# Optimization experiments

Hardware: AMD Instinct MI355X
Metric: run time of the kernel (lower is better)

## Reference

```python
import jax, jax.numpy as jnp
import numpy as np
import math

DIM = 1024
NUM_HEADS = 16
HEAD_DIM = 64
SEQ_LEN = 2048
ATTN_SCALE = 0.12


def cosine_norm(x, eps=1e-12):
    # unit-normalize along last dim
    return x * jax.lax.rsqrt(jnp.sum(x * x, axis=-1, keepdims=True) + eps)


def rotary_tables(T, head_dim):
    dim_quarter = max(1, head_dim // 4)
    angular_freq = (1.0 / 1024.0) ** jnp.linspace(0.0, 1.0, dim_quarter, dtype=jnp.float32)
    angular_freq = jnp.concatenate([angular_freq, jnp.zeros(dim_quarter, dtype=jnp.float32)])  # [head_dim//2]
    t = jnp.arange(T, dtype=jnp.float32)
    theta = t[:, None] * angular_freq[None, :]  # [T, head_dim//2]
    return jnp.cos(theta), jnp.sin(theta)


def apply_rotary(x_BTHD, cos, sin):
    # cos/sin: [T, head_dim//2] -> broadcast [1, T, 1, head_dim//2]
    c = cos[None, :, None, :]
    s = sin[None, :, None, :]
    x1, x2 = jnp.split(x_BTHD, 2, axis=-1)
    y1 = x1 * c + x2 * s
    y2 = -x1 * s + x2 * c
    return jnp.concatenate([y1, y2], axis=-1)


def setup_inputs() -> dict:
    key = jax.random.key(0)
    ks = jax.random.split(key, 6)
    x = jax.random.normal(ks[0], (1, SEQ_LEN, DIM), dtype=jnp.float32)
    init_std = 0.02
    Wq = jax.random.normal(ks[1], (DIM, NUM_HEADS * HEAD_DIM), dtype=jnp.float32) * init_std
    Wk = jax.random.normal(ks[2], (DIM, NUM_HEADS * HEAD_DIM), dtype=jnp.float32) * init_std
    Wv = jax.random.normal(ks[3], (DIM, NUM_HEADS * HEAD_DIM), dtype=jnp.float32) * init_std
    Wo = jax.random.normal(ks[4], (NUM_HEADS * HEAD_DIM, DIM), dtype=jnp.float32) * init_std
    # Scale param: initialized as ones * (1/sqrt(dim)); use rand around that magnitude
    s_qk = jax.random.uniform(ks[5], (NUM_HEADS, HEAD_DIM), dtype=jnp.float32,
                              minval=0.5, maxval=1.5) * (1.0 / math.sqrt(DIM))
    return {"x": x, "Wq": Wq, "Wk": Wk, "Wv": Wv, "Wo": Wo, "s_qk": s_qk}


def reference(x, Wq, Wk, Wv, Wo, s_qk):
    B, T, _ = x.shape
    # projections
    q = (x @ Wq).reshape(B, T, NUM_HEADS, HEAD_DIM)
    k = (x @ Wk).reshape(B, T, NUM_HEADS, HEAD_DIM)
    v = (x @ Wv).reshape(B, T, NUM_HEADS, HEAD_DIM)
    # effective scale: s * (init/scale) with init=1, scale=1/sqrt(dim)
    s_eff = s_qk * math.sqrt(DIM)  # [H, D]
    q = cosine_norm(q) * s_eff[None, None, :, :]
    k = cosine_norm(k) * s_eff[None, None, :, :]
    cos, sin = rotary_tables(T, HEAD_DIM)
    q = apply_rotary(q, cos, sin)
    k = apply_rotary(k, cos, sin)
    # causal attention with fixed scale 0.12 (block_mask == causal)
    scores = jnp.einsum('bthd,bshd->bhts', q, k) * ATTN_SCALE  # [B,H,T,T]
    causal = jnp.tril(jnp.ones((T, T), dtype=bool))
    scores = jnp.where(causal[None, None, :, :], scores, jnp.float32(-1e30))
    attn = jax.nn.softmax(scores, axis=-1)
    y = jnp.einsum('bhts,bshd->bthd', attn, v)
    y = y.reshape(B, T, NUM_HEADS * HEAD_DIM)
    return y @ Wo
```

## Files before the change

### kernel.cpp

```cpp
#include <hip/hip_runtime.h>

typedef unsigned short u16;
typedef unsigned int u32;
typedef __attribute__((ext_vector_type(8))) short bf16x8;
typedef __attribute__((ext_vector_type(4))) float f32x4;

__device__ __forceinline__ u16 f2bf(float x) {
  unsigned u = __float_as_uint(x);
  u += 0x7fffu + ((u >> 16) & 1u);
  return (u16)(u >> 16);
}
__device__ __forceinline__ float bf2f(u16 z) {
  return __uint_as_float((u32)z << 16);
}

__global__ __launch_bounds__(256) void prep(const float* __restrict__ x,
                                            const float* __restrict__ W0,
                                            const float* __restrict__ W1,
                                            const float* __restrict__ W2,
                                            const float* __restrict__ W3,
                                            u16* __restrict__ xb,
                                            u16* __restrict__ Wt,
                                            float2* __restrict__ rtab) {
  __shared__ alignas(16) u16 ls[64 * 72];
  int b = blockIdx.x;
  int tid = threadIdx.x;
  if (b < 2048) {
    int g = b * 256 + tid;
    int i = g * 4;
    float4 f = *(const float4*)(x + i);
    ushort4 o;
    o.x = f2bf(f.x); o.y = f2bf(f.y); o.z = f2bf(f.z); o.w = f2bf(f.w);
    *(ushort4*)(xb + i) = o;
    if (g < 2048 * 16) {
      int t = g >> 4, ii = g & 15;
      float fr = exp2f(-10.0f * (float)ii / 15.0f);
      float th = (float)t * fr;
      rtab[g] = make_float2(cosf(th), sinf(th));
    }
    return;
  }
  int bb = b - 2048;
  int z = bb >> 8;
  int rem = bb & 255;
  const float* W = (z == 0) ? W0 : (z == 1) ? W1 : (z == 2) ? W2 : W3;
  u16* o = Wt + (size_t)z * (1024u * 1024u);
  int kt = (rem >> 4) * 64, nt = (rem & 15) * 64;
  int r = tid >> 2, c0 = (tid & 3) * 16;
  const float* src = W + (size_t)(kt + r) * 1024 + nt + c0;
  u16 tmp[16];
#pragma unroll
  for (int c = 0; c < 16; c += 4) {
    float4 f = *(const float4*)(src + c);
    tmp[c + 0] = f2bf(f.x); tmp[c + 1] = f2bf(f.y);
    tmp[c + 2] = f2bf(f.z); tmp[c + 3] = f2bf(f.w);
  }
#pragma unroll
  for (int c = 0; c < 16; ++c) ls[r * 72 + c0 + c] = tmp[c];
  __syncthreads();
#pragma unroll
  for (int pass = 0; pass < 4; ++pass) {
    int n = pass * 16 + (tid >> 4);
    int kk = (tid & 15) * 4;
    ushort4 val;
    val.x = ls[(kk + 0) * 72 + n];
    val.y = ls[(kk + 1) * 72 + n];
    val.z = ls[(kk + 2) * 72 + n];
    val.w = ls[(kk + 3) * 72 + n];
    *(ushort4*)(o + (size_t)(nt + n) * 1024 + kt + kk) = val;
  }
}

#define GLD 40

__global__ __launch_bounds__(256) void gemm_qkv(const u16* __restrict__ A,
                                                const u16* __restrict__ Wt,
                                                u16* __restrict__ qb,
                                                u16* __restrict__ kb,
                                                u16* __restrict__ vt,
                                                const float* __restrict__ s_qk,
                                                const float2* __restrict__ rtab) {
  __shared__ alignas(16) u16 As[128 * GLD];
  __shared__ alignas(16) u16 Bs[128 * GLD];
  int z = blockIdx.z;
  const u16* B = Wt + (size_t)z * (1024u * 1024u);
  int tid = threadIdx.x;
  int bm = blockIdx.y * 128, bn = blockIdx.x * 128;
  int lane = tid & 63, w = tid >> 6;
  int wm = (w >> 1) * 64, wn = (w & 1) * 64;
  int m16 = lane & 15, q = lane >> 4;
  f32x4 acc[4][4] = {};
  int srow = tid >> 1, scol = (tid & 1) * 16;
  const u16* aptr = A + (size_t)(bm + srow) * 1024 + scol;
  const u16* bptr = B + (size_t)(bn + srow) * 1024 + scol;
  uint4 a0 = *(const uint4*)(aptr);
  uint4 a1 = *(const uint4*)(aptr + 8);
  uint4 b0 = *(const uint4*)(bptr);
  uint4 b1 = *(const uint4*)(bptr + 8);
  for (int k0 = 0; k0 < 1024; k0 += 32) {
    __syncthreads();
    *(uint4*)&As[srow * GLD + scol] = a0;
    *(uint4*)&As[srow * GLD + scol + 8] = a1;
    *(uint4*)&Bs[srow * GLD + scol] = b0;
    *(uint4*)&Bs[srow * GLD + scol + 8] = b1;
    uint4 na0, na1, nb0, nb1;
    if (k0 < 992) {
      na0 = *(const uint4*)(aptr + k0 + 32);
      na1 = *(const uint4*)(aptr + k0 + 40);
      nb0 = *(const uint4*)(bptr + k0 + 32);
      nb1 = *(const uint4*)(bptr + k0 + 40);
    }
    __syncthreads();
    bf16x8 af[4], bfr[4];
#pragma unroll
    for (int mt = 0; mt < 4; ++mt)
      af[mt] = *(const bf16x8*)&As[(wm + mt * 16 + m16) * GLD + q * 8];
#pragma unroll
    for (int nt = 0; nt < 4; ++nt)
      bfr[nt] = *(const bf16x8*)&Bs[(wn + nt * 16 + m16) * GLD + q * 8];
#pragma unroll
    for (int mt = 0; mt < 4; ++mt)
#pragma unroll
      for (int nt = 0; nt < 4; ++nt)
        acc[mt][nt] = __builtin_amdgcn_mfma_f32_16x16x32_bf16(af[mt], bfr[nt], acc[mt][nt], 0, 0, 0);
    if (k0 < 992) { a0 = na0; a1 = na1; b0 = nb0; b1 = nb1; }
  }
  int hh = (bn + wn) >> 6;
  if (z == 2) {
#pragma unroll
    for (int nt = 0; nt < 4; ++nt) {
      int n = bn + wn + nt * 16 + m16;
#pragma unroll
      for (int mt = 0; mt < 4; ++mt) {
        int t0 = bm + wm + mt * 16 + q * 4;
        ushort4 val;
        val.x = f2bf(acc[mt][nt][0]);
        val.y = f2bf(acc[mt][nt][1]);
        val.z = f2bf(acc[mt][nt][2]);
        val.w = f2bf(acc[mt][nt][3]);
        *(ushort4*)(vt + (size_t)n * 2048 + t0) = val;
      }
    }
  } else {
    u16* dst = z ? kb : qb;
    float se0 = s_qk[hh * 64 +  0 + m16] * 32.0f;
    float se1 = s_qk[hh * 64 + 16 + m16] * 32.0f;
    float se2 = s_qk[hh * 64 + 32 + m16] * 32.0f;
    float se3 = s_qk[hh * 64 + 48 + m16] * 32.0f;
#pragma unroll
    for (int mt = 0; mt < 4; ++mt)
#pragma unroll
      for (int r = 0; r < 4; ++r) {
        float ss = acc[mt][0][r] * acc[mt][0][r] + acc[mt][1][r] * acc[mt][1][r]
                 + acc[mt][2][r] * acc[mt][2][r] + acc[mt][3][r] * acc[mt][3][r];
        ss += __shfl_xor(ss, 1); ss += __shfl_xor(ss, 2);
        ss += __shfl_xor(ss, 4); ss += __shfl_xor(ss, 8);
        float inv = rsqrtf(ss + 1e-12f);
        int t = bm + wm + mt * 16 + q * 4 + r;
        float2 cs = rtab[t * 16 + m16];
        float x0 = acc[mt][0][r] * inv * se0;
        float x1 = acc[mt][1][r] * inv * se1;
        float x2 = acc[mt][2][r] * inv * se2;
        float x3 = acc[mt][3][r] * inv * se3;
        size_t off = (size_t)t * 1024 + hh * 64 + m16;
        dst[off]      = f2bf(x0 * cs.x + x2 * cs.y);
        dst[off + 16] = f2bf(x1);
        dst[off + 32] = f2bf(x2 * cs.x - x0 * cs.y);
        dst[off + 48] = f2bf(x3);
      }
  }
}

#define ALD 72
__global__ __launch_bounds__(256) void attn_flash(const u16* __restrict__ qb,
                                                  const u16* __restrict__ kb,
                                                  const u16* __restrict__ vt,
                                                  u16* __restrict__ yb) {
  __shared__ alignas(16) u16 Ks[64 * ALD];
  __shared__ alignas(16) u16 Vt[64 * ALD];
  __shared__ alignas(16) u16 Ps[4 * 16 * ALD];
  int h = blockIdx.x;
  int qt = 31 - blockIdx.y;
  int t0 = qt * 64;
  int tid = threadIdx.x;
  int lane = tid & 63, w = tid >> 6;
  int m16 = lane & 15, q = lane >> 4;
  int krow_s = tid >> 2, kcol_s = (tid & 3) * 16;
  const u16* kbase = kb + (size_t)krow_s * 1024 + h * 64 + kcol_s;
  const u16* vbase = vt + (size_t)(h * 64 + krow_s) * 2048 + kcol_s;
  u16* pw = &Ps[w * 16 * ALD];
  const u16* qrow = qb + (size_t)(t0 + w * 16 + m16) * 1024 + h * 64;
  bf16x8 qa0 = *(const bf16x8*)(qrow + q * 8);
  bf16x8 qa1 = *(const bf16x8*)(qrow + 32 + q * 8);
  f32x4 Yacc[4] = {};
  float lsum[4] = {0.f, 0.f, 0.f, 0.f};
  int trow = t0 + w * 16 + q * 4;
  uint4 kv0 = *(const uint4*)kbase;
  uint4 kv1 = *(const uint4*)(kbase + 8);
  uint4 vv0 = *(const uint4*)vbase;
  uint4 vv1 = *(const uint4*)(vbase + 8);
  for (int jt = 0; jt <= qt; ++jt) {
    __syncthreads();
    *(uint4*)&Ks[krow_s * ALD + kcol_s] = kv0;
    *(uint4*)&Ks[krow_s * ALD + kcol_s + 8] = kv1;
    *(uint4*)&Vt[krow_s * ALD + kcol_s] = vv0;
    *(uint4*)&Vt[krow_s * ALD + kcol_s + 8] = vv1;
    uint4 kn0, kn1, vn0, vn1;
    if (jt < qt) {
      const u16* kp = kbase + (size_t)(jt + 1) * 65536;
      const u16* vp = vbase + (jt + 1) * 64;
      kn0 = *(const uint4*)kp;
      kn1 = *(const uint4*)(kp + 8);
      vn0 = *(const uint4*)vp;
      vn1 = *(const uint4*)(vp + 8);
    }
    __syncthreads();
    f32x4 S[4] = {};
#pragma unroll
    for (int nt = 0; nt < 4; ++nt) {
      bf16x8 b0 = *(const bf16x8*)&Ks[(nt * 16 + m16) * ALD + q * 8];
      bf16x8 b1 = *(const bf16x8*)&Ks[(nt * 16 + m16) * ALD + 32 + q * 8];
      S[nt] = __builtin_amdgcn_mfma_f32_16x16x32_bf16(qa0, b0, S[nt], 0, 0, 0);
      S[nt] = __builtin_amdgcn_mfma_f32_16x16x32_bf16(qa1, b1, S[nt], 0, 0, 0);
    }
    bool diag = (jt == qt);
    int j0 = jt * 64;
    float tmp[4] = {0.f, 0.f, 0.f, 0.f};
#pragma unroll
    for (int nt = 0; nt < 4; ++nt) {
      int j = j0 + nt * 16 + m16;
#pragma unroll
      for (int r = 0; r < 4; ++r) {
        float p = __builtin_amdgcn_exp2f(S[nt][r] * 0.17312340490667562f);
        if (diag && (j > trow + r)) p = 0.f;
        tmp[r] += p;
        pw[(q * 4 + r) * ALD + nt * 16 + m16] = f2bf(p);
      }
    }
#pragma unroll
    for (int r = 0; r < 4; ++r) {
      float s = tmp[r];
      s += __shfl_xor(s, 1); s += __shfl_xor(s, 2);
      s += __shfl_xor(s, 4); s += __shfl_xor(s, 8);
      lsum[r] += s;
    }
    bf16x8 pa0 = *(const bf16x8*)&pw[m16 * ALD + q * 8];
    bf16x8 pa1 = *(const bf16x8*)&pw[m16 * ALD + 32 + q * 8];
#pragma unroll
    for (int nt = 0; nt < 4; ++nt) {
      bf16x8 b0 = *(const bf16x8*)&Vt[(nt * 16 + m16) * ALD + q * 8];
      bf16x8 b1 = *(const bf16x8*)&Vt[(nt * 16 + m16) * ALD + 32 + q * 8];
      Yacc[nt] = __builtin_amdgcn_mfma_f32_16x16x32_bf16(pa0, b0, Yacc[nt], 0, 0, 0);
      Yacc[nt] = __builtin_amdgcn_mfma_f32_16x16x32_bf16(pa1, b1, Yacc[nt], 0, 0, 0);
    }
    if (jt < qt) { kv0 = kn0; kv1 = kn1; vv0 = vn0; vv1 = vn1; }
  }
#pragma unroll
  for (int r = 0; r < 4; ++r) {
    float inv = __builtin_amdgcn_rcpf(lsum[r]);
    int t = t0 + w * 16 + q * 4 + r;
#pragma unroll
    for (int nt = 0; nt < 4; ++nt)
      yb[(size_t)t * 1024 + h * 64 + nt * 16 + m16] = f2bf(Yacc[nt][r] * inv);
  }
}

__global__ __launch_bounds__(256) void gemm_o(const u16* __restrict__ A,
                                              const u16* __restrict__ B,
                                              float* __restrict__ C) {
  __shared__ alignas(16) u16 As[128 * GLD];
  __shared__ alignas(16) u16 Bs[64 * GLD];
  int tid = threadIdx.x;
  int bm = blockIdx.y * 128, bn = blockIdx.x * 64;
  int lane = tid & 63, w = tid >> 6;
  int wm = w * 32;
  int m16 = lane & 15, q = lane >> 4;
  f32x4 acc[2][4] = {};
  int srA = tid >> 1, scA = (tid & 1) * 16;
  int srB = tid >> 2, scB = (tid & 3) * 8;
  const u16* aptr = A + (size_t)(bm + srA) * 1024 + scA;
  const u16* bptr = B + (size_t)(bn + srB) * 1024 + scB;
  uint4 a0 = *(const uint4*)(aptr);
  uint4 a1 = *(const uint4*)(aptr + 8);
  uint4 b0 = *(const uint4*)(bptr);
  for (int k0 = 0; k0 < 1024; k0 += 32) {
    __syncthreads();
    *(uint4*)&As[srA * GLD + scA] = a0;
    *(uint4*)&As[srA * GLD + scA + 8] = a1;
    *(uint4*)&Bs[srB * GLD + scB] = b0;
    uint4 na0, na1, nb0;
    if (k0 < 992) {
      na0 = *(const uint4*)(aptr + k0 + 32);
      na1 = *(const uint4*)(aptr + k0 + 40);
      nb0 = *(const uint4*)(bptr + k0 + 32);
    }
    __syncthreads();
    bf16x8 af[2], bfr[4];
#pragma unroll
    for (int mt = 0; mt < 2; ++mt)
      af[mt] = *(const bf16x8*)&As[(wm + mt * 16 + m16) * GLD + q * 8];
#pragma unroll
    for (int nt = 0; nt < 4; ++nt)
      bfr[nt] = *(const bf16x8*)&Bs[(nt * 16 + m16) * GLD + q * 8];
#pragma unroll
    for (int mt = 0; mt < 2; ++mt)
#pragma unroll
      for (int nt = 0; nt < 4; ++nt)
        acc[mt][nt] = __builtin_amdgcn_mfma_f32_16x16x32_bf16(af[mt], bfr[nt], acc[mt][nt], 0, 0, 0);
    if (k0 < 992) { a0 = na0; a1 = na1; b0 = nb0; }
  }
#pragma unroll
  for (int mt = 0; mt < 2; ++mt)
#pragma unroll
    for (int nt = 0; nt < 4; ++nt)
#pragma unroll
      for (int r = 0; r < 4; ++r) {
        int row = bm + wm + mt * 16 + q * 4 + r;
        int col = bn + nt * 16 + m16;
        C[(size_t)row * 1024 + col] = acc[mt][nt][r];
      }
}

extern "C" void kernel_launch(void* const* d_in, const int* in_sizes, int n_in,
                              void* d_out, int out_size, void* d_ws, size_t ws_size,
                              hipStream_t stream) {
  const float* x   = (const float*)d_in[0];
  const float* Wq  = (const float*)d_in[1];
  const float* Wk  = (const float*)d_in[2];
  const float* Wv  = (const float*)d_in[3];
  const float* Wo  = (const float*)d_in[4];
  const float* sqk = (const float*)d_in[5];
  float* out = (float*)d_out;
  char* ws = (char*)d_ws;

  u16*    xb   = (u16*)ws;
  u16*    Wt   = (u16*)(ws + ((size_t)4 << 20));
  float2* rtab = (float2*)(ws + ((size_t)12 << 20));
  u16*    qb16 = (u16*)(ws + ((size_t)16 << 20));
  u16*    kb16 = (u16*)(ws + ((size_t)20 << 20));
  u16*    vt16 = (u16*)(ws + ((size_t)24 << 20));
  u16*    yb   = (u16*)(ws + ((size_t)28 << 20));
  u16*    Wto  = Wt + (size_t)3 * 1024 * 1024;

  prep<<<3072, 256, 0, stream>>>(x, Wq, Wk, Wv, Wo, xb, Wt, rtab);
  gemm_qkv<<<dim3(8, 16, 3), 256, 0, stream>>>(xb, Wt, qb16, kb16, vt16, sqk, rtab);
  attn_flash<<<dim3(16, 32), 256, 0, stream>>>(qb16, kb16, vt16, yb);
  gemm_o<<<dim3(16, 16), 256, 0, stream>>>(yb, Wto, out);
}
```

Measured before the change: 154.0 us.

## Compute transposed score tile so each lane owns one query row's keys

Swaps the MFMA operands so the score tile comes out transposed: each lane holds four consecutive keys for a single query row. The row sum then accumulates per lane with no per-tile shuffle reduction, and only one cross-lane reduction plus broadcast runs at the end. P is packed with v_cvt_pk_bf16_f32 and written to LDS as one 8-byte store instead of four scalar 2-byte stores. The causal mask compares against the query row directly, and the per-tile shuffles and scattered LDS writes are meant to be removed in the softmax inner loop.

Result: faster. 147.7 us (-4.1%).

```diff
diff --git a/kernel.cpp b/kernel.cpp
--- a/kernel.cpp
+++ b/kernel.cpp
@@ -12,6 +12,11 @@
 }
 __device__ __forceinline__ float bf2f(u16 z) {
   return __uint_as_float((u32)z << 16);
+}
+__device__ __forceinline__ u32 cvtpk(float lo, float hi) {
+  u32 r;
+  asm("v_cvt_pk_bf16_f32 %0, %1, %2" : "=v"(r) : "v"(lo), "v"(hi));
+  return r;
 }
 
 __global__ __launch_bounds__(256) void prep(const float* __restrict__ x,
@@ -189,12 +194,12 @@
   const u16* kbase = kb + (size_t)krow_s * 1024 + h * 64 + kcol_s;
   const u16* vbase = vt + (size_t)(h * 64 + krow_s) * 2048 + kcol_s;
   u16* pw = &Ps[w * 16 * ALD];
-  const u16* qrow = qb + (size_t)(t0 + w * 16 + m16) * 1024 + h * 64;
-  bf16x8 qa0 = *(const bf16x8*)(qrow + q * 8);
-  bf16x8 qa1 = *(const bf16x8*)(qrow + 32 + q * 8);
+  int qrow = t0 + w * 16 + m16;
+  const u16* qr = qb + (size_t)qrow * 1024 + h * 64;
+  bf16x8 qa0 = *(const bf16x8*)(qr + q * 8);
+  bf16x8 qa1 = *(const bf16x8*)(qr + 32 + q * 8);
   f32x4 Yacc[4] = {};
-  float lsum[4] = {0.f, 0.f, 0.f, 0.f};
-  int trow = t0 + w * 16 + q * 4;
+  float lsum = 0.f;
   uint4 kv0 = *(const uint4*)kbase;
   uint4 kv1 = *(const uint4*)(kbase + 8);
   uint4 vv0 = *(const uint4*)vbase;
@@ -215,34 +220,34 @@
       vn1 = *(const uint4*)(vp + 8);
     }
     __syncthreads();
-    f32x4 S[4] = {};
+    f32x4 ST[4] = {};
 #pragma unroll
     for (int nt = 0; nt < 4; ++nt) {
       bf16x8 b0 = *(const bf16x8*)&Ks[(nt * 16 + m16) * ALD + q * 8];
       bf16x8 b1 = *(const bf16x8*)&Ks[(nt * 16 + m16) * ALD + 32 + q * 8];
-      S[nt] = __builtin_amdgcn_mfma_f32_16x16x32_bf16(qa0, b0, S[nt], 0, 0, 0);
-      S[nt] = __builtin_amdgcn_mfma_f32_16x16x32_bf16(qa1, b1, S[nt], 0, 0, 0);
+      ST[nt] = __builtin_amdgcn_mfma_f32_16x16x32_bf16(b0, qa0, ST[nt], 0, 0, 0);
+      ST[nt] = __builtin_amdgcn_mfma_f32_16x16x32_bf16(b1, qa1, ST[nt], 0, 0, 0);
     }
     bool diag = (jt == qt);
     int j0 = jt * 64;
-    float tmp[4] = {0.f, 0.f, 0.f, 0.f};
 #pragma unroll
     for (int nt = 0; nt < 4; ++nt) {
-      int j = j0 + nt * 16 + m16;
-#pragma unroll
-      for (int r = 0; r < 4; ++r) {
-        float p = __builtin_amdgcn_exp2f(S[nt][r] * 0.17312340490667562f);
-        if (diag && (j > trow + r)) p = 0.f;
-        tmp[r] += p;
-        pw[(q * 4 + r) * ALD + nt * 16 + m16] = f2bf(p);
+      int jbase = j0 + nt * 16 + q * 4;
+      float p0 = __builtin_amdgcn_exp2f(ST[nt][0] * 0.17312340490667562f);
+      float p1 = __builtin_amdgcn_exp2f(ST[nt][1] * 0.17312340490667562f);
+      float p2 = __builtin_amdgcn_exp2f(ST[nt][2] * 0.17312340490667562f);
+      float p3 = __builtin_amdgcn_exp2f(ST[nt][3] * 0.17312340490667562f);
+      if (diag) {
+        p0 = (jbase + 0 <= qrow) ? p0 : 0.f;
+        p1 = (jbase + 1 <= qrow) ? p1 : 0.f;
+        p2 = (jbase + 2 <= qrow) ? p2 : 0.f;
+        p3 = (jbase + 3 <= qrow) ? p3 : 0.f;
       }
-    }
-#pragma unroll
-    for (int r = 0; r < 4; ++r) {
-      float s = tmp[r];
-      s += __shfl_xor(s, 1); s += __shfl_xor(s, 2);
-      s += __shfl_xor(s, 4); s += __shfl_xor(s, 8);
-      lsum[r] += s;
+      lsum += (p0 + p1) + (p2 + p3);
+      uint2 pk;
+      pk.x = cvtpk(p0, p1);
+      pk.y = cvtpk(p2, p3);
+      *(uint2*)&pw[m16 * ALD + nt * 16 + q * 4] = pk;
     }
     bf16x8 pa0 = *(const bf16x8*)&pw[m16 * ALD + q * 8];
     bf16x8 pa1 = *(const bf16x8*)&pw[m16 * ALD + 32 + q * 8];
@@ -255,9 +260,13 @@
     }
     if (jt < qt) { kv0 = kn0; kv1 = kn1; vv0 = vn0; vv1 = vn1; }
   }
+  float tot = lsum;
+  tot += __shfl_xor(tot, 16);
+  tot += __shfl_xor(tot, 32);
 #pragma unroll
   for (int r = 0; r < 4; ++r) {
-    float inv = __builtin_amdgcn_rcpf(lsum[r]);
+    float Ls = __shfl(tot, q * 4 + r);
+    float inv = __builtin_amdgcn_rcpf(Ls);
     int t = t0 + w * 16 + q * 4 + r;
 #pragma unroll
     for (int nt = 0; nt < 4; ++nt)
```

## Split attention keys across warps with register-resident K/V and cross-warp reduction

Applied to the files above, without the earlier changes.

Restructures the flash attention kernel so each warp owns a 32-key slice of a 128-key block and computes S^T for all 64 queries. K and V fragments are loaded straight from global memory into registers, which removes the shared-memory K/V staging and the two per-iteration block barriers. Partial outputs and row sums are then reduced across warps through shared memory at the end. Probabilities are packed with a v_cvt_pk_bf16_f32 instruction. The trade-off is much higher register use (16 accumulator tiles per warp), uncoalesced per-lane global loads, and a final cross-warp reduction. The causal tail is handled by masking the last 128-key block, which for even qt covers keys past the diagonal that are zeroed.

Measured after the change: 145.6 us. 5.5% less time.

```diff
diff --git a/kernel.cpp b/kernel.cpp
--- a/kernel.cpp
+++ b/kernel.cpp
@@ -12,6 +12,11 @@
 }
 __device__ __forceinline__ float bf2f(u16 z) {
   return __uint_as_float((u32)z << 16);
+}
+__device__ __forceinline__ u32 cvtpk(float lo, float hi) {
+  u32 r;
+  asm("v_cvt_pk_bf16_f32 %0, %1, %2" : "=v"(r) : "v"(lo), "v"(hi));
+  return r;
 }
 
 __global__ __launch_bounds__(256) void prep(const float* __restrict__ x,
@@ -171,97 +176,150 @@
   }
 }
 
-#define ALD 72
+#define PLD 40
+#define RPD 20
 __global__ __launch_bounds__(256) void attn_flash(const u16* __restrict__ qb,
                                                   const u16* __restrict__ kb,
                                                   const u16* __restrict__ vt,
                                                   u16* __restrict__ yb) {
-  __shared__ alignas(16) u16 Ks[64 * ALD];
-  __shared__ alignas(16) u16 Vt[64 * ALD];
-  __shared__ alignas(16) u16 Ps[4 * 16 * ALD];
+  __shared__ alignas(16) unsigned char smb[12 * 64 * RPD * 4 + 4 * 64 * 4];
   int h = blockIdx.x;
   int qt = 31 - blockIdx.y;
   int t0 = qt * 64;
   int tid = threadIdx.x;
   int lane = tid & 63, w = tid >> 6;
   int m16 = lane & 15, q = lane >> 4;
-  int krow_s = tid >> 2, kcol_s = (tid & 3) * 16;
-  const u16* kbase = kb + (size_t)krow_s * 1024 + h * 64 + kcol_s;
-  const u16* vbase = vt + (size_t)(h * 64 + krow_s) * 2048 + kcol_s;
-  u16* pw = &Ps[w * 16 * ALD];
-  const u16* qrow = qb + (size_t)(t0 + w * 16 + m16) * 1024 + h * 64;
-  bf16x8 qa0 = *(const bf16x8*)(qrow + q * 8);
-  bf16x8 qa1 = *(const bf16x8*)(qrow + 32 + q * 8);
-  f32x4 Yacc[4] = {};
+  u16* pw = (u16*)smb + w * 64 * PLD;
+  bf16x8 qa[4][2];
+#pragma unroll
+  for (int qn = 0; qn < 4; ++qn) {
+    const u16* qr = qb + (size_t)(t0 + qn * 16 + m16) * 1024 + h * 64;
+    qa[qn][0] = *(const bf16x8*)(qr + q * 8);
+    qa[qn][1] = *(const bf16x8*)(qr + 32 + q * 8);
+  }
+  int wk = w * 32;
+  const u16* kbase = kb + (size_t)(wk + m16) * 1024 + h * 64 + q * 8;
+  const u16* vbase = vt + (size_t)(h * 64 + m16) * 2048 + wk + q * 8;
+  f32x4 Yacc[4][4] = {};
   float lsum[4] = {0.f, 0.f, 0.f, 0.f};
-  int trow = t0 + w * 16 + q * 4;
-  uint4 kv0 = *(const uint4*)kbase;
-  uint4 kv1 = *(const uint4*)(kbase + 8);
-  uint4 vv0 = *(const uint4*)vbase;
-  uint4 vv1 = *(const uint4*)(vbase + 8);
-  for (int jt = 0; jt <= qt; ++jt) {
-    __syncthreads();
-    *(uint4*)&Ks[krow_s * ALD + kcol_s] = kv0;
-    *(uint4*)&Ks[krow_s * ALD + kcol_s + 8] = kv1;
-    *(uint4*)&Vt[krow_s * ALD + kcol_s] = vv0;
-    *(uint4*)&Vt[krow_s * ALD + kcol_s + 8] = vv1;
-    uint4 kn0, kn1, vn0, vn1;
-    if (jt < qt) {
-      const u16* kp = kbase + (size_t)(jt + 1) * 65536;
-      const u16* vp = vbase + (jt + 1) * 64;
-      kn0 = *(const uint4*)kp;
-      kn1 = *(const uint4*)(kp + 8);
-      vn0 = *(const uint4*)vp;
-      vn1 = *(const uint4*)(vp + 8);
-    }
-    __syncthreads();
-    f32x4 S[4] = {};
-#pragma unroll
-    for (int nt = 0; nt < 4; ++nt) {
-      bf16x8 b0 = *(const bf16x8*)&Ks[(nt * 16 + m16) * ALD + q * 8];
-      bf16x8 b1 = *(const bf16x8*)&Ks[(nt * 16 + m16) * ALD + 32 + q * 8];
-      S[nt] = __builtin_amdgcn_mfma_f32_16x16x32_bf16(qa0, b0, S[nt], 0, 0, 0);
-      S[nt] = __builtin_amdgcn_mfma_f32_16x16x32_bf16(qa1, b1, S[nt], 0, 0, 0);
-    }
-    bool diag = (jt == qt);
-    int j0 = jt * 64;
-    float tmp[4] = {0.f, 0.f, 0.f, 0.f};
-#pragma unroll
-    for (int nt = 0; nt < 4; ++nt) {
-      int j = j0 + nt * 16 + m16;
-#pragma unroll
-      for (int r = 0; r < 4; ++r) {
-        float p = __builtin_amdgcn_exp2f(S[nt][r] * 0.17312340490667562f);
-        if (diag && (j > trow + r)) p = 0.f;
-        tmp[r] += p;
-        pw[(q * 4 + r) * ALD + nt * 16 + m16] = f2bf(p);
+  int nkb = (qt + 2) >> 1;
+  bf16x8 kfr[2][2];
+#pragma unroll
+  for (int kt = 0; kt < 2; ++kt) {
+    kfr[kt][0] = *(const bf16x8*)(kbase + kt * 16384);
+    kfr[kt][1] = *(const bf16x8*)(kbase + kt * 16384 + 32);
+  }
+  for (int kbi = 0; kbi < nkb; ++kbi) {
+    int kb0 = kbi * 128;
+    bf16x8 vfr[4];
+#pragma unroll
+    for (int nt = 0; nt < 4; ++nt)
+      vfr[nt] = *(const bf16x8*)(vbase + (size_t)nt * 32768 + kb0);
+    f32x4 ST[2][4] = {};
+#pragma unroll
+    for (int kt = 0; kt < 2; ++kt)
+#pragma unroll
+      for (int qn = 0; qn < 4; ++qn) {
+        ST[kt][qn] = __builtin_amdgcn_mfma_f32_16x16x32_bf16(kfr[kt][0], qa[qn][0], ST[kt][qn], 0, 0, 0);
+        ST[kt][qn] = __builtin_amdgcn_mfma_f32_16x16x32_bf16(kfr[kt][1], qa[qn][1], ST[kt][qn], 0, 0, 0);
+      }
+    bf16x8 kn[2][2];
+    bool more = (kbi + 1 < nkb);
+    if (more) {
+      const u16* kp = kbase + (size_t)(kb0 + 128) * 1024;
+#pragma unroll
+      for (int kt = 0; kt < 2; ++kt) {
+        kn[kt][0] = *(const bf16x8*)(kp + kt * 16384);
+        kn[kt][1] = *(const bf16x8*)(kp + kt * 16384 + 32);
+      }
+    }
+    bool last = (kbi == nkb - 1);
+#pragma unroll
+    for (int kt = 0; kt < 2; ++kt) {
+      int keyb = kb0 + wk + kt * 16 + q * 4;
+#pragma unroll
+      for (int qn = 0; qn < 4; ++qn) {
+        int qr_ = t0 + qn * 16 + m16;
+        float p0 = __builtin_amdgcn_exp2f(ST[kt][qn][0] * 0.17312340490667562f);
+        float p1 = __builtin_amdgcn_exp2f(ST[kt][qn][1] * 0.17312340490667562f);
+        float p2 = __builtin_amdgcn_exp2f(ST[kt][qn][2] * 0.17312340490667562f);
+        float p3 = __builtin_amdgcn_exp2f(ST[kt][qn][3] * 0.17312340490667562f);
+        if (last) {
+          p0 = (keyb + 0 <= qr_) ? p0 : 0.f;
+          p1 = (keyb + 1 <= qr_) ? p1 : 0.f;
+          p2 = (keyb + 2 <= qr_) ? p2 : 0.f;
+          p3 = (keyb + 3 <= qr_) ? p3 : 0.f;
+        }
+        lsum[qn] += (p0 + p1) + (p2 + p3);
+        uint2 pk2;
+        pk2.x = cvtpk(p0, p1);
+        pk2.y = cvtpk(p2, p3);
+        *(uint2*)&pw[(qn * 16 + m16) * PLD + kt * 16 + q * 4] = pk2;
+      }
+    }
+    bf16x8 pa[4];
+#pragma unroll
+    for (int qn = 0; qn < 4; ++qn)
+      pa[qn] = *(const bf16x8*)&pw[(qn * 16 + m16) * PLD + q * 8];
+#pragma unroll
+    for (int qn = 0; qn < 4; ++qn)
+#pragma unroll
+      for (int nt = 0; nt < 4; ++nt)
+        Yacc[qn][nt] = __builtin_amdgcn_mfma_f32_16x16x32_bf16(pa[qn], vfr[nt], Yacc[qn][nt], 0, 0, 0);
+    if (more) {
+      kfr[0][0] = kn[0][0]; kfr[0][1] = kn[0][1];
+      kfr[1][0] = kn[1][0]; kfr[1][1] = kn[1][1];
+    }
+  }
+#pragma unroll
+  for (int qn = 0; qn < 4; ++qn) {
+    lsum[qn] += __shfl_xor(lsum[qn], 16);
+    lsum[qn] += __shfl_xor(lsum[qn], 32);
+  }
+  __syncthreads();
+  float* Yr = (float*)smb;
+  float* Lb = (float*)(smb + 12 * 64 * RPD * 4);
+  if (q == 0) {
+#pragma unroll
+    for (int qn = 0; qn < 4; ++qn) Lb[w * 64 + qn * 16 + m16] = lsum[qn];
+  }
+#pragma unroll
+  for (int qn = 0; qn < 4; ++qn) {
+    if (qn != w) {
+      int idx = w * 3 + (qn < w ? qn : qn - 1);
+      float* dst = Yr + idx * 64 * RPD;
+#pragma unroll
+      for (int nt = 0; nt < 4; ++nt)
+        *(f32x4*)&dst[(nt * 16 + m16) * RPD + q * 4] = Yacc[qn][nt];
+    }
+  }
+  __syncthreads();
+  float Lt[4];
+#pragma unroll
+  for (int r = 0; r < 4; ++r) {
+    int row = w * 16 + q * 4 + r;
+    Lt[r] = ((Lb[row] + Lb[64 + row]) + (Lb[128 + row] + Lb[192 + row]));
+  }
+#pragma unroll
+  for (int nt = 0; nt < 4; ++nt) {
+    f32x4 y = {0.f, 0.f, 0.f, 0.f};
+#pragma unroll
+    for (int qn = 0; qn < 4; ++qn)
+      if (qn == w) y = Yacc[qn][nt];
+#pragma unroll
+    for (int wp = 0; wp < 4; ++wp) {
+      if (wp != w) {
+        int idx = wp * 3 + (w < wp ? w : w - 1);
+        f32x4 o = *(const f32x4*)&Yr[idx * 64 * RPD + (nt * 16 + m16) * RPD + q * 4];
+        y += o;
       }
     }
 #pragma unroll
     for (int r = 0; r < 4; ++r) {
-      float s = tmp[r];
-      s += __shfl_xor(s, 1); s += __shfl_xor(s, 2);
-      s += __shfl_xor(s, 4); s += __shfl_xor(s, 8);
-      lsum[r] += s;
-    }
-    bf16x8 pa0 = *(const bf16x8*)&pw[m16 * ALD + q * 8];
-    bf16x8 pa1 = *(const bf16x8*)&pw[m16 * ALD + 32 + q * 8];
-#pragma unroll
-    for (int nt = 0; nt < 4; ++nt) {
-      bf16x8 b0 = *(const bf16x8*)&Vt[(nt * 16 + m16) * ALD + q * 8];
-      bf16x8 b1 = *(const bf16x8*)&Vt[(nt * 16 + m16) * ALD + 32 + q * 8];
-      Yacc[nt] = __builtin_amdgcn_mfma_f32_16x16x32_bf16(pa0, b0, Yacc[nt], 0, 0, 0);
-      Yacc[nt] = __builtin_amdgcn_mfma_f32_16x16x32_bf16(pa1, b1, Yacc[nt], 0, 0, 0);
-    }
-    if (jt < qt) { kv0 = kn0; kv1 = kn1; vv0 = vn0; vv1 = vn1; }
-  }
-#pragma unroll
-  for (int r = 0; r < 4; ++r) {
-    float inv = __builtin_amdgcn_rcpf(lsum[r]);
-    int t = t0 + w * 16 + q * 4 + r;
-#pragma unroll
-    for (int nt = 0; nt < 4; ++nt)
-      yb[(size_t)t * 1024 + h * 64 + nt * 16 + m16] = f2bf(Yacc[nt][r] * inv);
+      int t = t0 + w * 16 + q * 4 + r;
+      yb[(size_t)t * 1024 + h * 64 + nt * 16 + m16] =
+          f2bf(y[r] * __builtin_amdgcn_rcpf(Lt[r]));
+    }
   }
 }
 
```
